# Optimization experiments

Measured on AMD Instinct MI355X. Metric: run time of the kernel, lower is better.

The kernel has to match this reference:

```python
import jax, jax.numpy as jnp
import numpy as np
from jax import lax

NUM_HEADS = 8
DIM = 384
B, H, W = 4, 128, 128
NEG_INF = -1e30


def setup_inputs() -> dict:
    key = jax.random.key(0)
    ks = jax.random.split(key, 5)
    x = jax.random.normal(ks[0], (B, DIM, H, W), dtype=jnp.float32)
    qkv_w = jax.random.normal(ks[1], (3 * DIM, DIM), dtype=jnp.float32) * 0.02   # 1x1 conv weight
    dw_w = jax.random.normal(ks[2], (3 * DIM, 1, 3, 3), dtype=jnp.float32) * 0.02  # depthwise 3x3
    proj_w = jax.random.normal(ks[3], (DIM, DIM), dtype=jnp.float32) * 0.02     # 1x1 conv weight
    temperature = jnp.ones((NUM_HEADS, 1, 1), dtype=jnp.float32)
    a1 = jnp.array([0.2], dtype=jnp.float32)
    a2 = jnp.array([0.2], dtype=jnp.float32)
    a3 = jnp.array([0.2], dtype=jnp.float32)
    a4 = jnp.array([0.2], dtype=jnp.float32)
    return {"x": x, "qkv_w": qkv_w, "dw_w": dw_w, "proj_w": proj_w,
            "temperature": temperature, "a1": a1, "a2": a2, "a3": a3, "a4": a4}


def _topk_softmax(attn, k):
    # keep top-k along last dim, softmax over kept entries (threshold == k-th largest)
    thr = lax.top_k(attn, k)[0][..., -1:]
    return jax.nn.softmax(jnp.where(attn >= thr, attn, NEG_INF), axis=-1)


def reference(x, qkv_w, dw_w, proj_w, temperature, a1, a2, a3, a4):
    b, c, h, w = x.shape
    head = NUM_HEADS
    C = c // head          # per-head channel dim (48)
    n = h * w              # token dim

    qkv = jnp.einsum('bchw,oc->bohw', x, qkv_w)  # 1x1 conv, no bias
    qkv = lax.conv_general_dilated(
        qkv, dw_w, window_strides=(1, 1), padding='SAME',
        feature_group_count=3 * c,
        dimension_numbers=('NCHW', 'OIHW', 'NCHW'))  # depthwise 3x3
    q, k, v = jnp.split(qkv, 3, axis=1)

    def heads(t):
        return t.reshape(b, head, C, n)  # b head c (h w)
    q, k, v = heads(q), heads(k), heads(v)

    q = q / jnp.linalg.norm(q, axis=-1, keepdims=True)
    k = k / jnp.linalg.norm(k, axis=-1, keepdims=True)

    attn = jnp.einsum('bhcn,bhdn->bhcd', q, k) * temperature  # [b,head,C,C]

    ks = [int(C / 2), int(C * 2 / 3), int(C * 3 / 4), int(C * 4 / 5)]
    weights = [a1, a2, a3, a4]
    out = jnp.zeros_like(v)
    for kk, a in zip(ks, weights):
        p = _topk_softmax(attn, kk)
        out = out + a * jnp.einsum('bhcd,bhdn->bhcn', p, v)

    out = out.reshape(b, c, h, w)
    out = jnp.einsum('bchw,oc->bohw', out, proj_w)  # 1x1 conv project_out
    return out
```

## Files before the change

kernel.cpp:

```cpp
#include <hip/hip_runtime.h>

#define NHEADS 8
#define DIM 384
#define BB 4
#define HW 16384
#define CPH 48

typedef unsigned int u32;
typedef _Float16 f16x8 __attribute__((ext_vector_type(8)));
typedef _Float16 f16x4 __attribute__((ext_vector_type(4)));
typedef __attribute__((ext_vector_type(4))) float f32x4;

__device__ __forceinline__ float wave_min(float v) {
    #pragma unroll
    for (int off = 32; off; off >>= 1) v = fminf(v, __shfl_xor(v, off));
    return v;
}
__device__ __forceinline__ float wave_max(float v) {
    #pragma unroll
    for (int off = 32; off; off >>= 1) v = fmaxf(v, __shfl_xor(v, off));
    return v;
}
__device__ __forceinline__ float wave_sum(float v) {
    #pragma unroll
    for (int off = 32; off; off >>= 1) v += __shfl_xor(v, off);
    return v;
}

__device__ __forceinline__ u32 pack2h(float a, float b) {
    union { _Float16 h[2]; u32 u; } p;
    p.h[0] = (_Float16)a; p.h[1] = (_Float16)b;
    return p.u;
}

#define GLOBAL_TO_LDS16(gsrc, ldst)                                           \
    __builtin_amdgcn_global_load_lds(                                         \
        (const __attribute__((address_space(1))) u32*)(gsrc),                 \
        (__attribute__((address_space(3))) u32*)(ldst), 16, 0, 0)

__global__ void cvt_w(const float* __restrict__ a, _Float16* __restrict__ o, int n)
{
    const int i = blockIdx.x * 256 + threadIdx.x;
    if (i < n) o[i] = (_Float16)a[i];
}

__global__ __launch_bounds__(256) void transpose_cvt(
    const float* __restrict__ x, _Float16* __restrict__ xt)
{
    const int n0 = blockIdx.x * 64;
    const int c0 = blockIdx.y * 192;
    const int b  = blockIdx.z;
    __shared__ u32 tile[64 * 97];
    const int t = threadIdx.x, w = t >> 6, l = t & 63;

    const float* xb = x + ((size_t)b * DIM + c0) * HW + n0 + l;
    #pragma unroll 4
    for (int j = 0; j < 24; ++j) {
        const int cc = j * 8 + w * 2;
        const float v0 = xb[(size_t)cc * HW];
        const float v1 = xb[(size_t)(cc + 1) * HW];
        tile[l * 97 + (cc >> 1)] = pack2h(v0, v1);
    }
    __syncthreads();

    _Float16* ob = xt + ((size_t)b * HW + n0) * DIM + c0;
    #pragma unroll
    for (int it = 0; it < 6; ++it) {
        const int elem = it * 2048 + t * 8;
        const int nl = elem / 192, col = elem % 192;
        const int base = nl * 97 + (col >> 1);
        u32 out4[4] = { tile[base], tile[base + 1], tile[base + 2], tile[base + 3] };
        *(uint4*)&ob[(size_t)nl * DIM + col] = *(const uint4*)out4;
    }
}

__global__ __launch_bounds__(256) void transpose16(
    const _Float16* __restrict__ in, _Float16* __restrict__ ot)
{
    const int n0 = blockIdx.x * 128;
    const int c0 = blockIdx.y * 192;
    const int b  = blockIdx.z;
    __shared__ _Float16 tile[128 * 194];
    const int t = threadIdx.x, w = t >> 6, l = t & 63;

    const _Float16* ib = in + ((size_t)b * DIM + c0) * HW + n0 + 2 * l;
    #pragma unroll 4
    for (int j = 0; j < 48; ++j) {
        const int cc = j * 4 + w;
        union { u32 u; _Float16 h[2]; } v;
        v.u = *(const u32*)&ib[(size_t)cc * HW];
        tile[(2 * l) * 194 + cc]     = v.h[0];
        tile[(2 * l + 1) * 194 + cc] = v.h[1];
    }
    __syncthreads();

    _Float16* ob = ot + ((size_t)b * HW + n0) * DIM + c0;
    #pragma unroll
    for (int it = 0; it < 12; ++it) {
        const int elem = it * 2048 + t * 8;
        const int nl = elem / 192, col = elem % 192;
        const _Float16* src = &tile[nl * 194 + col];
        u32 out4[4];
        out4[0] = *(const u32*)&src[0];
        out4[1] = *(const u32*)&src[2];
        out4[2] = *(const u32*)&src[4];
        out4[3] = *(const u32*)&src[6];
        *(uint4*)&ob[(size_t)nl * DIM + col] = *(const uint4*)out4;
    }
}

__global__ __launch_bounds__(256) void gemm_f16(
    const _Float16* __restrict__ W, const _Float16* __restrict__ Xt,
    void* __restrict__ Y, int out_f32, int wbs)
{
    const int n0 = blockIdx.x * 128;
    const int m0 = blockIdx.y * 128;
    const int b  = blockIdx.z;
    const int M  = gridDim.y * 128;

    __shared__ _Float16 sA[128 * 32];
    __shared__ _Float16 sB[128 * 32];

    const int t = threadIdx.x;
    const int w = t >> 6;
    const int l = t & 63;

    const _Float16* gA = W + (size_t)b * wbs
                           + ((size_t)(m0 + w * 32 + (l >> 2))) * DIM + (l & 3) * 8;
    const _Float16* gB = Xt + ((size_t)b * HW + n0 + w * 32 + (l >> 2)) * DIM + (l & 3) * 8;
    _Float16* lA = &sA[(w * 32) * 32];
    _Float16* lB = &sB[(w * 32) * 32];

    f32x4 acc[4][4];
    #pragma unroll
    for (int i = 0; i < 4; ++i)
        #pragma unroll
        for (int j = 0; j < 4; ++j)
            acc[i][j] = (f32x4){0.f, 0.f, 0.f, 0.f};

    const int wm = (w >> 1) * 64, wn = (w & 1) * 64;
    const int fr = l & 15, fk = (l >> 4) * 8;

    for (int k0 = 0; k0 < DIM; k0 += 32) {
        __syncthreads();
        GLOBAL_TO_LDS16(gA + k0,             lA);
        GLOBAL_TO_LDS16(gA + k0 + 16 * DIM,  lA + 16 * 32);
        GLOBAL_TO_LDS16(gB + k0,             lB);
        GLOBAL_TO_LDS16(gB + k0 + 16 * DIM,  lB + 16 * 32);
        __syncthreads();

        f16x8 af[4], bfv[4];
        #pragma unroll
        for (int mi = 0; mi < 4; ++mi)
            af[mi] = *(const f16x8*)&sA[(wm + mi * 16 + fr) * 32 + fk];
        #pragma unroll
        for (int ni = 0; ni < 4; ++ni)
            bfv[ni] = *(const f16x8*)&sB[(wn + ni * 16 + fr) * 32 + fk];
        #pragma unroll
        for (int mi = 0; mi < 4; ++mi)
            #pragma unroll
            for (int ni = 0; ni < 4; ++ni)
                acc[mi][ni] = __builtin_amdgcn_mfma_f32_16x16x32_f16(
                    af[mi], bfv[ni], acc[mi][ni], 0, 0, 0);
    }

    const int er = (l >> 4) * 4;
    if (out_f32) {
        float* Yp = (float*)Y + (size_t)b * M * HW;
        #pragma unroll
        for (int mi = 0; mi < 4; ++mi)
            #pragma unroll
            for (int ni = 0; ni < 4; ++ni)
                #pragma unroll
                for (int r = 0; r < 4; ++r)
                    Yp[(size_t)(m0 + wm + mi * 16 + er + r) * HW + n0 + wn + ni * 16 + fr]
                        = acc[mi][ni][r];
    } else {
        _Float16* Yp = (_Float16*)Y + (size_t)b * M * HW;
        #pragma unroll
        for (int mi = 0; mi < 4; ++mi)
            #pragma unroll
            for (int ni = 0; ni < 4; ++ni)
                #pragma unroll
                for (int r = 0; r < 4; ++r)
                    Yp[(size_t)(m0 + wm + mi * 16 + er + r) * HW + n0 + wn + ni * 16 + fr]
                        = (_Float16)acc[mi][ni][r];
    }
}

__global__ __launch_bounds__(256) void dwconv_all(
    const _Float16* __restrict__ in, const float* __restrict__ w9,
    _Float16* __restrict__ oq, _Float16* __restrict__ ok_,
    _Float16* __restrict__ ov, float* __restrict__ ss)
{
    const int j  = blockIdx.x & 3;
    const int p  = blockIdx.x >> 2;
    const int c  = p % 1152;
    const int b  = p / 1152;
    const int r0 = j * 32;

    __shared__ __align__(16) _Float16 tile[34 * 136 + 8];
    const int t = threadIdx.x;

    const uint4 z4 = make_uint4(0, 0, 0, 0);
    for (int i = t; i < 579; i += 256)
        *(uint4*)&tile[i * 8] = z4;
    __syncthreads();

    const _Float16* ip = in + (size_t)p * HW;
    for (int cc = t; cc < 34 * 16; cc += 256) {
        const int i = cc >> 4, seg = cc & 15;
        const int g = r0 - 1 + i;
        if ((unsigned)g < 128u)
            *(f16x8*)&tile[i * 136 + 8 + seg * 8] = *(const f16x8*)&ip[g * 128 + seg * 8];
    }

    float w[9];
    #pragma unroll
    for (int i = 0; i < 9; ++i) w[i] = w9[c * 9 + i];
    __syncthreads();

    const int yr = t >> 3;
    const int xc = (t & 7) * 16;

    float acc[16];
    #pragma unroll
    for (int cc = 0; cc < 16; ++cc) acc[cc] = 0.f;

    #pragma unroll
    for (int dy = 0; dy < 3; ++dy) {
        const _Float16* rp = &tile[(yr + dy) * 136 + xc];
        const f16x8 v0 = *(const f16x8*)&rp[0];
        const f16x8 v1 = *(const f16x8*)&rp[8];
        const f16x8 v2 = *(const f16x8*)&rp[16];
        const f16x8 v3 = *(const f16x8*)&rp[24];
        float rv[18];
        #pragma unroll
        for (int i = 0; i < 18; ++i) {
            const int idx = 7 + i;
            const _Float16 h = (idx < 8)  ? v0[idx]
                             : (idx < 16) ? v1[idx - 8]
                             : (idx < 24) ? v2[idx - 16]
                                          : v3[idx - 24];
            rv[i] = (float)h;
        }
        const float w0 = w[dy * 3 + 0], w1 = w[dy * 3 + 1], w2 = w[dy * 3 + 2];
        #pragma unroll
        for (int cc = 0; cc < 16; ++cc) {
            acc[cc] = fmaf(rv[cc],     w0, acc[cc]);
            acc[cc] = fmaf(rv[cc + 1], w1, acc[cc]);
            acc[cc] = fmaf(rv[cc + 2], w2, acc[cc]);
        }
    }

    alignas(16) _Float16 oh[16];
    float ssum = 0.f;
    #pragma unroll
    for (int cc = 0; cc < 16; ++cc) {
        oh[cc] = (_Float16)acc[cc];
        ssum = fmaf(acc[cc], acc[cc], ssum);
    }
    const int grp = c / 384;
    const int cl  = c - grp * 384;
    _Float16* obase = (grp == 0) ? oq : (grp == 1) ? ok_ : ov;
    _Float16* op = obase + ((size_t)b * DIM + cl) * HW + (r0 + yr) * 128 + xc;
    *(f16x8*)&op[0] = *(const f16x8*)&oh[0];
    *(f16x8*)&op[8] = *(const f16x8*)&oh[8];

    if (c < 768) {
        __syncthreads();
        float* red = (float*)tile;
        red[t] = ssum;
        __syncthreads();
        for (int s = 128; s > 0; s >>= 1) {
            if (t < s) red[t] += red[t + s];
            __syncthreads();
        }
        if (t == 0) atomicAdd(&ss[b * (2 * DIM) + c], red[0]);
    }
}

#define GNC 1024
__global__ __launch_bounds__(256) void gram_qk(
    const _Float16* __restrict__ qA, const _Float16* __restrict__ kA,
    float* __restrict__ G)
{
    const int n0 = blockIdx.x * GNC;
    const int h  = blockIdx.y;
    const int b  = blockIdx.z;
    const _Float16* qb = qA + ((size_t)b * DIM + h * CPH) * HW + n0;
    const _Float16* kb = kA + ((size_t)b * DIM + h * CPH) * HW + n0;

    const int t = threadIdx.x;
    const int w = t >> 6, l = t & 63;
    const int fr = l & 15, fk = (l >> 4) * 8;

    f32x4 acc[3][3];
    #pragma unroll
    for (int i = 0; i < 3; ++i)
        #pragma unroll
        for (int j = 0; j < 3; ++j)
            acc[i][j] = (f32x4){0.f, 0.f, 0.f, 0.f};

    const int nbase = w * (GNC / 4);
    #pragma unroll 4
    for (int nn = 0; nn < GNC / 4; nn += 32) {
        f16x8 qf[3], kf[3];
        #pragma unroll
        for (int i = 0; i < 3; ++i) {
            const size_t off = (size_t)(i * 16 + fr) * HW + nbase + nn + fk;
            qf[i] = *(const f16x8*)&qb[off];
            kf[i] = *(const f16x8*)&kb[off];
        }
        #pragma unroll
        for (int i = 0; i < 3; ++i)
            #pragma unroll
            for (int j = 0; j < 3; ++j)
                acc[i][j] = __builtin_amdgcn_mfma_f32_16x16x32_f16(
                    qf[i], kf[j], acc[i][j], 0, 0, 0);
    }

    __shared__ float red[4][CPH * CPH];
    const int er = (l >> 4) * 4;
    #pragma unroll
    for (int i = 0; i < 3; ++i)
        #pragma unroll
        for (int j = 0; j < 3; ++j)
            #pragma unroll
            for (int r = 0; r < 4; ++r)
                red[w][(i * 16 + er + r) * CPH + j * 16 + fr] = acc[i][j][r];
    __syncthreads();

    float* Gp = G + ((size_t)(b * NHEADS + h)) * CPH * CPH;
    for (int i = t; i < CPH * CPH; i += 256)
        atomicAdd(&Gp[i], red[0][i] + red[1][i] + red[2][i] + red[3][i]);
}

__global__ __launch_bounds__(64) void topk_combine(
    const float* __restrict__ G, const float* __restrict__ ss,
    const float* __restrict__ temp,
    const float* __restrict__ a1, const float* __restrict__ a2,
    const float* __restrict__ a3, const float* __restrict__ a4,
    float* __restrict__ P)
{
    const int row = blockIdx.x;
    const int bh  = row / CPH;
    const int r   = row - bh * CPH;
    const int b = bh >> 3, h = bh & 7;
    const int l = threadIdx.x;

    const float tpr = temp[h];
    const float* ssb = ss + b * (2 * DIM);
    const float invq = 1.f / sqrtf(ssb[h * CPH + r]);

    float att = -3.0e38f;
    if (l < CPH)
        att = G[(size_t)row * CPH + l] * invq * (1.f / sqrtf(ssb[DIM + h * CPH + l])) * tpr;

    int cnt = 0;
    #pragma unroll
    for (int i = 0; i < CPH; ++i)
        cnt += (__shfl(att, i) > att) ? 1 : 0;

    const float mx   = wave_max(att);
    const float thr0 = wave_min((l < CPH && cnt < 24) ? att : 3.0e38f);
    const float thr1 = wave_min((l < CPH && cnt < 32) ? att : 3.0e38f);
    const float thr2 = wave_min((l < CPH && cnt < 36) ? att : 3.0e38f);
    const float thr3 = wave_min((l < CPH && cnt < 38) ? att : 3.0e38f);

    const float e = (l < CPH) ? expf(att - mx) : 0.f;
    const float Z0 = wave_sum(att >= thr0 ? e : 0.f);
    const float Z1 = wave_sum(att >= thr1 ? e : 0.f);
    const float Z2 = wave_sum(att >= thr2 ? e : 0.f);
    const float Z3 = wave_sum(att >= thr3 ? e : 0.f);

    const float w0 = a1[0] / Z0, w1 = a2[0] / Z1, w2 = a3[0] / Z2, w3 = a4[0] / Z3;
    float pv = 0.f;
    if (att >= thr0) pv += w0 * e;
    if (att >= thr1) pv += w1 * e;
    if (att >= thr2) pv += w2 * e;
    if (att >= thr3) pv += w3 * e;
    if (l < CPH) P[(size_t)row * CPH + l] = pv;
}

__global__ __launch_bounds__(256) void fuse_pw(
    const float* __restrict__ pw, const float* __restrict__ P,
    _Float16* __restrict__ Wf)
{
    const int o0 = blockIdx.x * CPH;
    const int h  = blockIdx.y;
    const int b  = blockIdx.z;
    const int t  = threadIdx.x;

    __shared__ float sP[CPH][CPH];
    __shared__ float sW[CPH][CPH + 1];
    for (int i = t; i < CPH * CPH; i += 256) {
        const int r = i / CPH, cc = i % CPH;
        sP[r][cc] = P[((size_t)(b * NHEADS + h)) * CPH * CPH + i];
        sW[r][cc] = pw[(size_t)(o0 + r) * DIM + h * CPH + cc];
    }
    __syncthreads();

    for (int i = t; i < CPH * CPH; i += 256) {
        const int o = i / CPH, d = i % CPH;
        float s = 0.f;
        #pragma unroll
        for (int c = 0; c < CPH; ++c)
            s = fmaf(sW[o][c], sP[c][d], s);
        Wf[((size_t)b * DIM + o0 + o) * DIM + h * CPH + d] = (_Float16)s;
    }
}

extern "C" void kernel_launch(void* const* d_in, const int* in_sizes, int n_in,
                              void* d_out, int out_size, void* d_ws, size_t ws_size,
                              hipStream_t stream)
{
    const float* x      = (const float*)d_in[0];
    const float* qkv_w  = (const float*)d_in[1];
    const float* dw_w   = (const float*)d_in[2];
    const float* proj_w = (const float*)d_in[3];
    const float* temp   = (const float*)d_in[4];
    const float* a1 = (const float*)d_in[5];
    const float* a2 = (const float*)d_in[6];
    const float* a3 = (const float*)d_in[7];
    const float* a4 = (const float*)d_in[8];
    float* out = (float*)d_out;

    const size_t PBE = (size_t)HW * DIM;
    const size_t WQE = (size_t)1152 * 384;
    const size_t WPE = (size_t)384 * 384;

    auto need_for = [&](size_t nb) -> size_t {
        return nb * PBE * 2 * 7 + (WQE + nb * WPE) * 2
             + (nb * 768 + 2 * nb * NHEADS * CPH * CPH) * 4;
    };

    int nb, npass;
    if      (ws_size >= need_for(4)) { nb = 4; npass = 1; }
    else if (ws_size >= need_for(2)) { nb = 2; npass = 2; }
    else if (ws_size >= need_for(1)) { nb = 1; npass = 4; }
    else return;

    _Float16* A  = (_Float16*)d_ws;
    _Float16* C  = A + (size_t)nb * PBE;
    _Float16* D  = C + (size_t)3 * nb * PBE;
    _Float16* E  = D + (size_t)nb * PBE;
    _Float16* F  = E + (size_t)nb * PBE;
    _Float16* wq = F + (size_t)nb * PBE;
    _Float16* Wf = wq + WQE;
    float* buf_ss = (float*)(Wf + (size_t)nb * WPE);
    float* buf_G  = buf_ss + (size_t)nb * 768;
    float* buf_P  = buf_G + (size_t)nb * NHEADS * CPH * CPH;

    cvt_w<<<dim3((1152 * 384 + 255) / 256), 256, 0, stream>>>(qkv_w, wq, 1152 * 384);

    for (int p = 0; p < npass; ++p) {
        const int b0 = p * nb;
        const float* xp   = x   + (size_t)b0 * PBE;
        float*       outp = out + (size_t)b0 * PBE;

        transpose_cvt<<<dim3(HW / 64, 2, nb), 256, 0, stream>>>(xp, A);
        hipMemsetAsync(buf_ss, 0,
                       ((size_t)nb * 768 + (size_t)nb * NHEADS * CPH * CPH) * sizeof(float),
                       stream);

        gemm_f16<<<dim3(HW / 128, 1152 / 128, nb), 256, 0, stream>>>(wq, A, C, 0, 0);

        dwconv_all<<<dim3(nb * 1152 * 4), 256, 0, stream>>>(C, dw_w, D, E, F, buf_ss);

        gram_qk<<<dim3(HW / GNC, NHEADS, nb), 256, 0, stream>>>(D, E, buf_G);
        topk_combine<<<dim3(nb * NHEADS * CPH), 64, 0, stream>>>(
            buf_G, buf_ss, temp, a1, a2, a3, a4, buf_P);

        fuse_pw<<<dim3(DIM / CPH, NHEADS, nb), 256, 0, stream>>>(proj_w, buf_P, Wf);

        transpose16<<<dim3(HW / 128, 2, nb), 256, 0, stream>>>(F, A);

        gemm_f16<<<dim3(HW / 128, DIM / 128, nb), 256, 0, stream>>>(Wf, A, outp, 1, (int)WPE);
    }
}
```

Baseline: 459.3 us.

## Load GEMM fragments directly from global memory and remap workgroups for locality

```diff
diff --git a/kernel.cpp b/kernel.cpp
--- a/kernel.cpp
+++ b/kernel.cpp
@@ -32,11 +32,6 @@
     p.h[0] = (_Float16)a; p.h[1] = (_Float16)b;
     return p.u;
 }
-
-#define GLOBAL_TO_LDS16(gsrc, ldst)                                           \
-    __builtin_amdgcn_global_load_lds(                                         \
-        (const __attribute__((address_space(1))) u32*)(gsrc),                 \
-        (__attribute__((address_space(3))) u32*)(ldst), 16, 0, 0)
 
 __global__ void cvt_w(const float* __restrict__ a, _Float16* __restrict__ o, int n)
 {
@@ -113,23 +108,23 @@
     const _Float16* __restrict__ W, const _Float16* __restrict__ Xt,
     void* __restrict__ Y, int out_f32, int wbs)
 {
-    const int n0 = blockIdx.x * 128;
-    const int m0 = blockIdx.y * 128;
-    const int b  = blockIdx.z;
-    const int M  = gridDim.y * 128;
-
-    __shared__ _Float16 sA[128 * 32];
-    __shared__ _Float16 sB[128 * 32];
+    const int nwg    = gridDim.x;
+    const int mtiles = nwg >> 7;
+    const int bid    = blockIdx.x;
+    const int wg     = (bid & 7) * (nwg >> 3) + (bid >> 3);
+    const int m0     = (wg % mtiles) * 128;
+    const int n0     = (wg / mtiles) * 128;
+    const int b      = blockIdx.z;
+    const int M      = mtiles * 128;
 
     const int t = threadIdx.x;
     const int w = t >> 6;
     const int l = t & 63;
-
-    const _Float16* gA = W + (size_t)b * wbs
-                           + ((size_t)(m0 + w * 32 + (l >> 2))) * DIM + (l & 3) * 8;
-    const _Float16* gB = Xt + ((size_t)b * HW + n0 + w * 32 + (l >> 2)) * DIM + (l & 3) * 8;
-    _Float16* lA = &sA[(w * 32) * 32];
-    _Float16* lB = &sB[(w * 32) * 32];
+    const int wm = (w >> 1) * 64, wn = (w & 1) * 64;
+    const int fr = l & 15, fk = (l >> 4) * 8;
+
+    const _Float16* Ab = W + (size_t)b * wbs + ((size_t)m0 + wm + fr) * DIM + fk;
+    const _Float16* Bb = Xt + ((size_t)b * HW + n0 + wn + fr) * DIM + fk;
 
     f32x4 acc[4][4];
     #pragma unroll
@@ -138,30 +133,21 @@
         for (int j = 0; j < 4; ++j)
             acc[i][j] = (f32x4){0.f, 0.f, 0.f, 0.f};
 
-    const int wm = (w >> 1) * 64, wn = (w & 1) * 64;
-    const int fr = l & 15, fk = (l >> 4) * 8;
-
+    #pragma unroll 4
     for (int k0 = 0; k0 < DIM; k0 += 32) {
-        __syncthreads();
-        GLOBAL_TO_LDS16(gA + k0,             lA);
-        GLOBAL_TO_LDS16(gA + k0 + 16 * DIM,  lA + 16 * 32);
-        GLOBAL_TO_LDS16(gB + k0,             lB);
-        GLOBAL_TO_LDS16(gB + k0 + 16 * DIM,  lB + 16 * 32);
-        __syncthreads();
-
-        f16x8 af[4], bfv[4];
+        f16x8 af[4], bf[4];
         #pragma unroll
         for (int mi = 0; mi < 4; ++mi)
-            af[mi] = *(const f16x8*)&sA[(wm + mi * 16 + fr) * 32 + fk];
+            af[mi] = *(const f16x8*)&Ab[(size_t)(mi * 16) * DIM + k0];
         #pragma unroll
         for (int ni = 0; ni < 4; ++ni)
-            bfv[ni] = *(const f16x8*)&sB[(wn + ni * 16 + fr) * 32 + fk];
+            bf[ni] = *(const f16x8*)&Bb[(size_t)(ni * 16) * DIM + k0];
         #pragma unroll
         for (int mi = 0; mi < 4; ++mi)
             #pragma unroll
             for (int ni = 0; ni < 4; ++ni)
                 acc[mi][ni] = __builtin_amdgcn_mfma_f32_16x16x32_f16(
-                    af[mi], bfv[ni], acc[mi][ni], 0, 0, 0);
+                    af[mi], bf[ni], acc[mi][ni], 0, 0, 0);
     }
 
     const int er = (l >> 4) * 4;
@@ -464,7 +450,7 @@
                        ((size_t)nb * 768 + (size_t)nb * NHEADS * CPH * CPH) * sizeof(float),
                        stream);
 
-        gemm_f16<<<dim3(HW / 128, 1152 / 128, nb), 256, 0, stream>>>(wq, A, C, 0, 0);
+        gemm_f16<<<dim3((1152 / 128) * (HW / 128), 1, nb), 256, 0, stream>>>(wq, A, C, 0, 0);
 
         dwconv_all<<<dim3(nb * 1152 * 4), 256, 0, stream>>>(C, dw_w, D, E, F, buf_ss);
 
@@ -476,6 +462,6 @@
 
         transpose16<<<dim3(HW / 128, 2, nb), 256, 0, stream>>>(F, A);
 
-        gemm_f16<<<dim3(HW / 128, DIM / 128, nb), 256, 0, stream>>>(Wf, A, outp, 1, (int)WPE);
-    }
-}
+        gemm_f16<<<dim3((DIM / 128) * (HW / 128), 1, nb), 256, 0, stream>>>(Wf, A, outp, 1, (int)WPE);
+    }
+}
```

New measurement: 599.0 us. 1.3x slower.
